# Kernel optimization log

Hardware: AMD Instinct MI355X
Metric: run time of the kernel (lower is better)

Reference implementation:

```python
import jax, jax.numpy as jnp
import numpy as np

EPS = 1e-10


def setup_inputs() -> dict:
    key = jax.random.key(0)
    kx, ky = jax.random.split(key)
    x = jax.random.normal(kx, (8, 8192, 3), dtype=jnp.float32)
    y = jax.random.normal(ky, (8, 8192, 3), dtype=jnp.float32)
    return {"x": x, "y": y}


def reference(x, y):
    # x: (B, N, 3), y: (B, M, 3)
    xy = -2.0 * jnp.einsum("bnd,bmd->bnm", x, y)          # (B, N, M)
    xx = jnp.sum(x * x, axis=-1, keepdims=True)            # (B, N, 1)
    yy = jnp.sum(y * y, axis=-1, keepdims=True)            # (B, M, 1)
    dist = jnp.sqrt(xy + xx + jnp.swapaxes(yy, 1, 2) + EPS)  # (B, N, M)
    distance1 = jnp.min(dist, axis=2)                      # (B, N): x -> nearest y
    distance2 = jnp.min(dist, axis=1)                      # (B, M): y -> nearest x
    mean1 = jnp.mean(distance1, axis=-1)                   # (B,)
    mean2 = jnp.mean(distance2, axis=-1)                   # (B,)
    return jnp.sum(jnp.maximum(mean1, mean2))
```

## Files before the change

kernel.cpp:

```cpp
#include <hip/hip_runtime.h>


#define BB 8
#define NN 8192
#define NPTS (BB*NN)
#define BLK 256
#define CCOLS 128
#define CT 4
#define RT 2
#define STRIPS 32
#define GRID 1024

typedef __attribute__((ext_vector_type(8))) short bf16x8;
typedef __attribute__((ext_vector_type(16))) float f32x16;

__device__ __forceinline__ unsigned f2mono(float f) {
    unsigned u = __float_as_uint(f);
    return u ^ ((unsigned)((int)u >> 31) | 0x80000000u);
}
__device__ __forceinline__ float mono2f(unsigned m) {
    unsigned u = ((int)m >= 0) ? ~m : (m ^ 0x80000000u);
    return __uint_as_float(u);
}
__device__ __forceinline__ unsigned bfh(float v) {
    unsigned u = __float_as_uint(v);
    u += 0x7FFFu + ((u >> 16) & 1u);
    return u >> 16;
}
__device__ __forceinline__ float bff(unsigned h) {
    return __uint_as_float(h << 16);
}
__device__ __forceinline__ unsigned pk(unsigned lo, unsigned hi) {
    return (lo & 0xFFFFu) | (hi << 16);
}

__global__ void prep_kernel(const float* __restrict__ x, const float* __restrict__ y,
                            uint4* __restrict__ afr, uint4* __restrict__ bfr,
                            unsigned* __restrict__ counter) {
    int i = blockIdx.x * BLK + threadIdx.x;
    if (i == 0) *counter = 0;
    const float* src = (i < NPTS) ? x : y;
    int j = (i < NPTS) ? i : i - NPTS;
    float c0 = src[3*j], c1 = src[3*j+1], c2 = src[3*j+2];
    float s2 = c0*c0 + c1*c1 + c2*c2;
    unsigned sh = bfh(s2), sl = bfh(s2 - bff(sh));
    float a0 = -2.f*c0, a1 = -2.f*c1, a2 = -2.f*c2;
    unsigned ah0 = bfh(a0), ah1 = bfh(a1), ah2 = bfh(a2);
    unsigned al0 = bfh(a0 - bff(ah0)), al1 = bfh(a1 - bff(ah1)), al2 = bfh(a2 - bff(ah2));
    unsigned bh0 = bfh(c0), bh1 = bfh(c1), bh2 = bfh(c2);
    unsigned bl0 = bfh(c0 - bff(bh0)), bl1 = bfh(c1 - bff(bh1)), bl2 = bfh(c2 - bff(bh2));
    const unsigned one = 0x3F80u;
    afr[2*i]   = make_uint4(pk(ah0,ah1), pk(ah2,al0), pk(al1,al2), pk(ah0,ah1));
    afr[2*i+1] = make_uint4(pk(ah2,sh),  pk(sl,one),  pk(one,0u),  0u);
    bfr[2*i]   = make_uint4(pk(bh0,bh1), pk(bh2,bh0), pk(bh1,bh2), pk(bl0,bl1));
    bfr[2*i+1] = make_uint4(pk(bl2,one), pk(one,sh),  pk(sl,0u),   0u);
}

__device__ __forceinline__ bf16x8 cvt(uint4 v) { return __builtin_bit_cast(bf16x8, v); }

__global__ __launch_bounds__(BLK, 4) void
main_kernel(const uint4* __restrict__ afr, const uint4* __restrict__ bfr,
            float* __restrict__ bpart, unsigned* __restrict__ counter,
            float* __restrict__ out) {
    __shared__ unsigned colmin[CCOLS];
    __shared__ float red[4];
    __shared__ float gg[8];
    __shared__ int lastflag;
    const int bi  = blockIdx.x;
    const int dir = bi >> 9;
    const int b   = (bi >> 6) & 7;
    const int cc  = bi & 63;
    const uint4* Af = afr + (dir ? 2*NPTS : 0);
    const uint4* Bf = bfr + (dir ? 0 : 2*NPTS);
    const int tid = threadIdx.x;
    const int lane = tid & 63, w = tid >> 6;
    const int m = lane & 31;
    const int hb = lane >> 5;

    if (tid < CCOLS) colmin[tid] = 0xFFFFFFFFu;

    bf16x8 bf[CT];
#pragma unroll
    for (int ct = 0; ct < CT; ++ct) {
        int c = b * NN + cc * CCOLS + ct * 32 + m;
        bf[ct] = cvt(Bf[2*c + hb]);
    }

    f32x16 zro;
#pragma unroll
    for (int i = 0; i < 16; ++i) zro[i] = 0.f;

    float rm[CT];
#pragma unroll
    for (int ct = 0; ct < CT; ++ct) rm[ct] = 3.4e38f;

    const int rowbase = b * NN + w * 64 + m;
    uint4 cur[RT], nxt[RT];
#pragma unroll
    for (int t = 0; t < RT; ++t) cur[t] = Af[2*(rowbase + t*32) + hb];

#pragma unroll 1
    for (int s = 0; s < STRIPS; ++s) {
        const int np = (s + 1 < STRIPS) ? (s + 1) : s;
#pragma unroll
        for (int t = 0; t < RT; ++t) nxt[t] = Af[2*(rowbase + np*256 + t*32) + hb];
        bf16x8 ca = cvt(cur[0]), cb = cvt(cur[1]);
#pragma unroll
        for (int ct = 0; ct < CT; ++ct) {
            f32x16 a0 = __builtin_amdgcn_mfma_f32_32x32x16_bf16(ca, bf[ct], zro, 0, 0, 0);
            f32x16 a1 = __builtin_amdgcn_mfma_f32_32x32x16_bf16(cb, bf[ct], zro, 0, 0, 0);
            float m0 = fminf(fminf(a0[0], a1[0]), rm[ct]);
            float m1 = fminf(a0[1], a1[1]);
            float m2 = fminf(a0[2], a1[2]);
            float m3 = fminf(a0[3], a1[3]);
#pragma unroll
            for (int r = 4; r < 16; r += 4) {
                m0 = fminf(fminf(a0[r],   a1[r]),   m0);
                m1 = fminf(fminf(a0[r+1], a1[r+1]), m1);
                m2 = fminf(fminf(a0[r+2], a1[r+2]), m2);
                m3 = fminf(fminf(a0[r+3], a1[r+3]), m3);
            }
            rm[ct] = fminf(fminf(m0, m1), fminf(m2, m3));
        }
#pragma unroll
        for (int t = 0; t < RT; ++t) cur[t] = nxt[t];
    }

#pragma unroll
    for (int ct = 0; ct < CT; ++ct) {
        float p = fminf(rm[ct], __shfl_xor(rm[ct], 32, 64));
        if (hb == 0) atomicMin(&colmin[ct * 32 + m], f2mono(p));
    }
    __syncthreads();

    float d = (tid < CCOLS) ? sqrtf(fmaxf(mono2f(colmin[tid]), 0.f) + 1e-10f) : 0.f;
#pragma unroll
    for (int off = 32; off; off >>= 1) d += __shfl_down(d, off, 64);
    if (lane == 0) red[w] = d;
    __syncthreads();
    if (tid == 0) {
        float total = red[0] + red[1] + red[2] + red[3];
        atomicExch(&bpart[bi], total);
        __threadfence();
        unsigned old = atomicAdd(counter, 1u);
        lastflag = (old == (GRID - 1));
    }
    __syncthreads();

    if (lastflag) {
        float v0 = atomicAdd(&bpart[2*tid], 0.f) + atomicAdd(&bpart[2*tid+1], 0.f);
        float v1 = atomicAdd(&bpart[512 + 2*tid], 0.f) + atomicAdd(&bpart[512 + 2*tid+1], 0.f);
#pragma unroll
        for (int off = 16; off; off >>= 1) {
            v0 += __shfl_down(v0, off, 32);
            v1 += __shfl_down(v1, off, 32);
        }
        if ((tid & 31) == 0) gg[tid >> 5] = fmaxf(v0, v1);
        __syncthreads();
        if (tid == 0) {
            float acc = 0.f;
#pragma unroll
            for (int k = 0; k < 8; ++k) acc += gg[k];
            out[0] = acc * (1.0f / (float)NN);
        }
    }
}

extern "C" void kernel_launch(void* const* d_in, const int* in_sizes, int n_in,
                              void* d_out, int out_size, void* d_ws, size_t ws_size,
                              hipStream_t stream) {
    const float* x = (const float*)d_in[0];
    const float* y = (const float*)d_in[1];
    float* out = (float*)d_out;

    char* ws = (char*)d_ws;
    uint4* afr = (uint4*)ws;
    uint4* bfr = afr + 4 * NPTS;
    float* bpart = (float*)(bfr + 4 * NPTS);
    unsigned* counter = (unsigned*)(bpart + GRID);

    prep_kernel<<<(2 * NPTS) / BLK, BLK, 0, stream>>>(x, y, afr, bfr, counter);
    main_kernel<<<GRID, BLK, 0, stream>>>(afr, bfr, bpart, counter, out);
}
```

Measured before the change: 117.6 us.

## Hand-schedule MFMA and min3 reductions with inline asm and sched barriers

Replaces the compiler-scheduled MFMA loop with inline-asm MFMAs rotating through three accumulators. Each tile's min-reduction runs with v_min3_f32 while the next MFMA is in flight, and sched_barrier fences hold that order. The next strip's loads move after the first MFMAs. The goal is to hide MFMA latency behind VALU work and cut the number of min instructions. Inline asm hides the dependencies from the compiler, so the MFMA-to-VALU hazard handling and register pressure become risks.

```diff
diff --git a/kernel.cpp b/kernel.cpp
--- a/kernel.cpp
+++ b/kernel.cpp
@@ -58,6 +58,27 @@
 
 __device__ __forceinline__ bf16x8 cvt(uint4 v) { return __builtin_bit_cast(bf16x8, v); }
 
+#define SB() __builtin_amdgcn_sched_barrier(0)
+
+#define MFMA_V(D, A, B)                                                        \
+    asm("v_mfma_f32_32x32x16_bf16 %0, %1, %2, %3"                              \
+        : "=&v"(D) : "v"(A), "v"(B), "v"(zro))
+
+#define MIN3(d, a, b, c)                                                       \
+    asm("v_min3_f32 %0, %1, %2, %3" : "=v"(d) : "v"(a), "v"(b), "v"(c))
+
+#define RED16(P, RM) do {                                                      \
+    float q0_, q1_, q2_, q3_, q4_, u0_, u1_;                                   \
+    MIN3(q0_, P[0],  P[1],  P[2]);                                             \
+    MIN3(q1_, P[3],  P[4],  P[5]);                                             \
+    MIN3(q2_, P[6],  P[7],  P[8]);                                             \
+    MIN3(q3_, P[9],  P[10], P[11]);                                            \
+    MIN3(q4_, P[12], P[13], P[14]);                                            \
+    MIN3(u0_, q0_, q1_, q2_);                                                  \
+    MIN3(u1_, q3_, q4_, P[15]);                                                \
+    MIN3(RM, u0_, u1_, RM);                                                    \
+} while (0)
+
 __global__ __launch_bounds__(BLK, 4) void
 main_kernel(const uint4* __restrict__ afr, const uint4* __restrict__ bfr,
             float* __restrict__ bpart, unsigned* __restrict__ counter,
@@ -94,36 +115,37 @@
 #pragma unroll
     for (int ct = 0; ct < CT; ++ct) rm[ct] = 3.4e38f;
 
-    const int rowbase = b * NN + w * 64 + m;
-    uint4 cur[RT], nxt[RT];
-#pragma unroll
-    for (int t = 0; t < RT; ++t) cur[t] = Af[2*(rowbase + t*32) + hb];
+    const uint4* Afp = Af + (2 * (b * NN + w * 64 + m) + hb);
+    uint4 cur0 = Afp[0], cur1 = Afp[64];
 
 #pragma unroll 1
     for (int s = 0; s < STRIPS; ++s) {
         const int np = (s + 1 < STRIPS) ? (s + 1) : s;
-#pragma unroll
-        for (int t = 0; t < RT; ++t) nxt[t] = Af[2*(rowbase + np*256 + t*32) + hb];
-        bf16x8 ca = cvt(cur[0]), cb = cvt(cur[1]);
-#pragma unroll
-        for (int ct = 0; ct < CT; ++ct) {
-            f32x16 a0 = __builtin_amdgcn_mfma_f32_32x32x16_bf16(ca, bf[ct], zro, 0, 0, 0);
-            f32x16 a1 = __builtin_amdgcn_mfma_f32_32x32x16_bf16(cb, bf[ct], zro, 0, 0, 0);
-            float m0 = fminf(fminf(a0[0], a1[0]), rm[ct]);
-            float m1 = fminf(a0[1], a1[1]);
-            float m2 = fminf(a0[2], a1[2]);
-            float m3 = fminf(a0[3], a1[3]);
-#pragma unroll
-            for (int r = 4; r < 16; r += 4) {
-                m0 = fminf(fminf(a0[r],   a1[r]),   m0);
-                m1 = fminf(fminf(a0[r+1], a1[r+1]), m1);
-                m2 = fminf(fminf(a0[r+2], a1[r+2]), m2);
-                m3 = fminf(fminf(a0[r+3], a1[r+3]), m3);
-            }
-            rm[ct] = fminf(fminf(m0, m1), fminf(m2, m3));
-        }
-#pragma unroll
-        for (int t = 0; t < RT; ++t) cur[t] = nxt[t];
+        const bf16x8 A0 = cvt(cur0), A1 = cvt(cur1);
+
+        f32x16 p0, p1, p2;
+        MFMA_V(p0, A0, bf[0]);
+        MFMA_V(p1, A1, bf[0]);
+        MFMA_V(p2, A0, bf[1]);
+        uint4 nxt0 = Afp[np * 512];
+        uint4 nxt1 = Afp[np * 512 + 64];
+        SB();
+        RED16(p0, rm[0]);  MFMA_V(p0, A1, bf[1]);
+        SB();
+        RED16(p1, rm[0]);  MFMA_V(p1, A0, bf[2]);
+        SB();
+        RED16(p2, rm[1]);  MFMA_V(p2, A1, bf[2]);
+        SB();
+        RED16(p0, rm[1]);  MFMA_V(p0, A0, bf[3]);
+        SB();
+        RED16(p1, rm[2]);  MFMA_V(p1, A1, bf[3]);
+        SB();
+        RED16(p2, rm[2]);
+        SB();
+        RED16(p0, rm[3]);
+        RED16(p1, rm[3]);
+
+        cur0 = nxt0; cur1 = nxt1;
     }
 
 #pragma unroll
```

Result: faster. 111.9 us (-4.8%).
